# Performance work log

Hardware: AMD Instinct MI355X
Metric: run time of the kernel (lower is better)

The kernel has to match this reference:

```python
import jax, jax.numpy as jnp
import numpy as np

HD, M = 4096, 14336

def setup_inputs() -> dict:
    key = jax.random.key(0)
    k_x, k_g, k_u, k_d = jax.random.split(key, 4)
    scale = 1.0 / np.sqrt(HD)
    x = jax.random.normal(k_x, (4, 2048, HD), dtype=jnp.float16)
    # Dequantized fp16 weights, stored torch-style as [out_features, in_features]
    W_gate = (jax.random.normal(k_g, (M, HD), dtype=jnp.float16) * jnp.float16(scale))
    W_up   = (jax.random.normal(k_u, (M, HD), dtype=jnp.float16) * jnp.float16(scale))
    W_down = (jax.random.normal(k_d, (HD, M), dtype=jnp.float16) * jnp.float16(1.0 / np.sqrt(M)))
    return {"x": x, "W_gate": W_gate, "W_up": W_up, "W_down": W_down}

def reference(x, W_gate, W_up, W_down):
    # SwiGLU: down( silu(x @ Wg^T) * (x @ Wu^T) )
    gate = jnp.einsum("bsh,mh->bsm", x, W_gate)   # [B,S,M]
    up = jnp.einsum("bsh,mh->bsm", x, W_up)       # [B,S,M]
    h = jax.nn.silu(gate) * up                       # fused elementwise
    out = jnp.einsum("bsm,hm->bsh", h, W_down)    # [B,S,HD]
    return out
```

## Files before the change

kernel.cpp:

```cpp
#include <hip/hip_runtime.h>

typedef _Float16 f16;
typedef _Float16 f16x8 __attribute__((ext_vector_type(8)));
typedef float f32x4 __attribute__((ext_vector_type(4)));

__device__ __forceinline__ f16x8 cvt8(f32x4 lo, f32x4 hi) {
    f16x8 h;
    h[0] = (f16)lo[0]; h[1] = (f16)lo[1]; h[2] = (f16)lo[2]; h[3] = (f16)lo[3];
    h[4] = (f16)hi[0]; h[5] = (f16)hi[1]; h[6] = (f16)hi[2]; h[7] = (f16)hi[3];
    return h;
}

__global__ __launch_bounds__(256)
void cvt_f32_f16(const float* __restrict__ in, f16* __restrict__ out, long long n) {
    long long i = ((long long)blockIdx.x * 256 + threadIdx.x) * 8;
    const long long stride = (long long)gridDim.x * 256 * 8;
    for (; i < n; i += stride) {
        f32x4 a = *(const f32x4*)(in + i);
        f32x4 b = *(const f32x4*)(in + i + 4);
        *(f16x8*)(out + i) = cvt8(a, b);
    }
}

__global__ void fill_sentinel_f32(float* __restrict__ out, long long n) {
    long long i = (long long)blockIdx.x * blockDim.x + threadIdx.x;
    long long stride = (long long)gridDim.x * blockDim.x;
    for (; i < n; i += stride) out[i] = 1.0f;
}

__device__ __forceinline__ void gload_lds16(const f16* g, f16* l) {
    __builtin_amdgcn_global_load_lds(
        (const __attribute__((address_space(1))) unsigned int*)(unsigned long long)g,
        (__attribute__((address_space(3))) unsigned int*)(unsigned int)(unsigned long long)l,
        16, 0, 0);
}

template<int EPI>
__global__ __launch_bounds__(512, 2)
void mlp_gemm16c(const f16* __restrict__ A, const f16* __restrict__ B0,
                 void* __restrict__ Cv, int K, int ldc,
                 int nRow, int nCol, int RG) {
    __shared__ __align__(16) f16 smA[3][256 * 32];
    __shared__ __align__(16) f16 smB0[3][256 * 32];

    const int lin   = blockIdx.x;
    const int perSg = RG * nCol;
    const int sg    = lin / perSg;
    const int rem   = lin - sg * perSg;
    int rgIn = nRow - sg * RG; if (rgIn > RG) rgIn = RG;
    const int colB = rem / rgIn;
    const int rowB = sg * RG + (rem - colB * rgIn);

    const long long blockRow = (long long)rowB * 256;
    const long long blockCol = (long long)colB * 256;

    const int tid  = threadIdx.x;
    const int w    = tid >> 6;
    const int lane = tid & 63;
    const int waveM = w >> 2;
    const int waveN = w & 3;

    const int dr   = tid >> 2;
    const int dblk = tid & 3;
    const int gblk = (dblk - (dr >> 1)) & 3;
    const f16* gA0  = A  + (blockRow + dr) * (long long)K + gblk * 8;
    const f16* gA1  = gA0 + 128 * (long long)K;
    const f16* gB0a = B0 + (blockCol + dr) * (long long)K + gblk * 8;
    const f16* gB0b = gB0a + 128 * (long long)K;
    const int wbase = w * 512;

    const int fr = lane & 15;
    const int hi = lane >> 4;
    int aOff[8], bOff[4];
#pragma unroll
    for (int i = 0; i < 8; ++i) {
        const int r = waveM * 128 + i * 16 + fr;
        aOff[i] = r * 32 + (((hi + (r >> 1)) & 3) << 3);
    }
#pragma unroll
    for (int n = 0; n < 4; ++n) {
        const int r = waveN * 64 + n * 16 + fr;
        bOff[n] = r * 32 + (((hi + (r >> 1)) & 3) << 3);
    }

    f32x4 acc0[8][4];
#pragma unroll
    for (int mi = 0; mi < 8; ++mi)
#pragma unroll
        for (int ni = 0; ni < 4; ++ni)
            acc0[mi][ni] = (f32x4){0.f, 0.f, 0.f, 0.f};

    auto stage = [&](int b) {
        gload_lds16(gA0,  &smA[b][wbase]);           gA0  += 32;
        gload_lds16(gA1,  &smA[b][4096 + wbase]);    gA1  += 32;
        gload_lds16(gB0a, &smB0[b][wbase]);          gB0a += 32;
        gload_lds16(gB0b, &smB0[b][4096 + wbase]);   gB0b += 32;
    };

    auto compute = [&](int b) {
        f16x8 aF[8], bF[4];
#pragma unroll
        for (int i = 0; i < 8; ++i) aF[i] = *(const f16x8*)(&smA[b][aOff[i]]);
#pragma unroll
        for (int n = 0; n < 4; ++n) bF[n] = *(const f16x8*)(&smB0[b][bOff[n]]);
#pragma unroll
        for (int mi = 0; mi < 8; ++mi)
#pragma unroll
            for (int ni = 0; ni < 4; ++ni)
                acc0[mi][ni] = __builtin_amdgcn_mfma_f32_16x16x32_f16(
                    aF[mi], bF[ni], acc0[mi][ni], 0, 0, 0);
    };

    const int nk = K >> 5;
    stage(0);
    stage(1);
    int cur = 0;
    for (int t = 0; t < nk - 1; ++t) {
        asm volatile("s_waitcnt vmcnt(4)" ::: "memory");
        __builtin_amdgcn_s_barrier();
        __builtin_amdgcn_sched_barrier(0);
        if (t + 2 < nk) {
            int nb = cur + 2; if (nb >= 3) nb -= 3;
            stage(nb);
        }
        compute(cur);
        cur = (cur == 2) ? 0 : cur + 1;
    }
    asm volatile("s_waitcnt vmcnt(0)" ::: "memory");
    __builtin_amdgcn_s_barrier();
    __builtin_amdgcn_sched_barrier(0);
    compute(cur);

    const long long orBase = blockRow + waveM * 128 + hi * 4;
    const long long ocBase = blockCol + waveN * 64 + fr;
#pragma unroll
    for (int mi = 0; mi < 8; ++mi)
#pragma unroll
        for (int ni = 0; ni < 4; ++ni)
#pragma unroll
            for (int j = 0; j < 4; ++j) {
                const long long idx =
                    (orBase + mi * 16 + j) * (long long)ldc + (ocBase + ni * 16);
                float v = acc0[mi][ni][j];
                if constexpr (EPI == 0) {
                    ((float*)Cv)[idx] = v;
                } else if constexpr (EPI == 1) {
                    ((f16*)Cv)[idx] = (f16)(v / (1.f + __expf(-v)));
                } else {
                    f16* Hc = (f16*)Cv;
                    float h = (float)Hc[idx];
                    Hc[idx] = (f16)(h * v);
                }
            }
}

template<bool IS16>
__device__ __forceinline__ f16x8 load8(const char* p) {
    if constexpr (IS16) return *(const f16x8*)p;
    const float* f = (const float*)p;
    return cvt8(*(const f32x4*)f, *(const f32x4*)(f + 4));
}

template<bool FUSED, bool A16, bool B16>
__global__ __launch_bounds__(256)
void mlp_gemm(const void* __restrict__ Av, const void* __restrict__ B0v,
              const void* __restrict__ B1v, void* __restrict__ Cv,
              int K, int ldc, int nRow, int nCol, int RG) {
    __shared__ __align__(16) f16 smA[128 * 32];
    __shared__ __align__(16) f16 smB0[128 * 32];
    __shared__ __align__(16) f16 smB1[FUSED ? 128 * 32 : 8];

    const int lin   = blockIdx.x;
    const int perSg = RG * nCol;
    const int sg    = lin / perSg;
    const int rem   = lin - sg * perSg;
    int rgIn = nRow - sg * RG; if (rgIn > RG) rgIn = RG;
    const int colB = rem / rgIn;
    const int rowB = sg * RG + (rem - colB * rgIn);

    const long long blockRow = (long long)rowB * 128;
    const long long blockCol = (long long)colB * 128;

    const int tid  = threadIdx.x;
    const int w    = tid >> 6;
    const int lane = tid & 63;
    const int waveM = w >> 1;
    const int waveN = w & 1;

    const int r0 = tid >> 2;
    const int s0 = tid & 3;
    const int szA = A16 ? 2 : 4;
    const int szB = B16 ? 2 : 4;
    const char* gA0  = (const char*)Av  + ((blockRow + r0)      * (long long)K + s0 * 8) * szA;
    const char* gA1  = (const char*)Av  + ((blockRow + r0 + 64) * (long long)K + s0 * 8) * szA;
    const char* gB00 = (const char*)B0v + ((blockCol + r0)      * (long long)K + s0 * 8) * szB;
    const char* gB01 = (const char*)B0v + ((blockCol + r0 + 64) * (long long)K + s0 * 8) * szB;
    const char* gB10 = FUSED ? (const char*)B1v + ((blockCol + r0)      * (long long)K + s0 * 8) * szB : nullptr;
    const char* gB11 = FUSED ? (const char*)B1v + ((blockCol + r0 + 64) * (long long)K + s0 * 8) * szB : nullptr;

    const int off0 = tid * 8;
    const int off1 = off0 + 2048;

    const int fr = lane & 15;
    const int fk = (lane >> 4) * 8;
    int offA[4], offB[4];
#pragma unroll
    for (int i = 0; i < 4; ++i) {
        offA[i] = (waveM * 64 + i * 16 + fr) * 32 + fk;
        offB[i] = (waveN * 64 + i * 16 + fr) * 32 + fk;
    }

    f32x4 acc0[4][4];
    f32x4 acc1[4][4];
#pragma unroll
    for (int mi = 0; mi < 4; ++mi)
#pragma unroll
        for (int ni = 0; ni < 4; ++ni) {
            acc0[mi][ni] = (f32x4){0.f, 0.f, 0.f, 0.f};
            if constexpr (FUSED) acc1[mi][ni] = (f32x4){0.f, 0.f, 0.f, 0.f};
        }

    const int ksteps = K >> 5;
    for (int kt = 0; kt < ksteps; ++kt) {
        f16x8 vA0  = load8<A16>(gA0);
        f16x8 vA1  = load8<A16>(gA1);
        f16x8 vB00 = load8<B16>(gB00);
        f16x8 vB01 = load8<B16>(gB01);
        f16x8 vB10, vB11;
        if constexpr (FUSED) {
            vB10 = load8<B16>(gB10);
            vB11 = load8<B16>(gB11);
        }
        gA0 += 32 * szA; gA1 += 32 * szA;
        gB00 += 32 * szB; gB01 += 32 * szB;
        if constexpr (FUSED) { gB10 += 32 * szB; gB11 += 32 * szB; }

        __syncthreads();

        *(f16x8*)(smA  + off0) = vA0;
        *(f16x8*)(smA  + off1) = vA1;
        *(f16x8*)(smB0 + off0) = vB00;
        *(f16x8*)(smB0 + off1) = vB01;
        if constexpr (FUSED) {
            *(f16x8*)(smB1 + off0) = vB10;
            *(f16x8*)(smB1 + off1) = vB11;
        }

        __syncthreads();

        f16x8 aF[4], bF[4], b1F[4];
#pragma unroll
        for (int i = 0; i < 4; ++i) aF[i] = *(const f16x8*)(smA + offA[i]);
#pragma unroll
        for (int i = 0; i < 4; ++i) bF[i] = *(const f16x8*)(smB0 + offB[i]);
        if constexpr (FUSED) {
#pragma unroll
            for (int i = 0; i < 4; ++i) b1F[i] = *(const f16x8*)(smB1 + offB[i]);
        }

#pragma unroll
        for (int mi = 0; mi < 4; ++mi)
#pragma unroll
            for (int ni = 0; ni < 4; ++ni) {
                acc0[mi][ni] = __builtin_amdgcn_mfma_f32_16x16x32_f16(
                    aF[mi], bF[ni], acc0[mi][ni], 0, 0, 0);
                if constexpr (FUSED)
                    acc1[mi][ni] = __builtin_amdgcn_mfma_f32_16x16x32_f16(
                        aF[mi], b1F[ni], acc1[mi][ni], 0, 0, 0);
            }
    }

    const long long orBase = blockRow + waveM * 64 + ((lane >> 4) * 4);
    const long long ocBase = blockCol + waveN * 64 + fr;
#pragma unroll
    for (int mi = 0; mi < 4; ++mi)
#pragma unroll
        for (int ni = 0; ni < 4; ++ni)
#pragma unroll
            for (int j = 0; j < 4; ++j) {
                const long long idx =
                    (orBase + mi * 16 + j) * (long long)ldc + (ocBase + ni * 16);
                if constexpr (FUSED) {
                    float gv = acc0[mi][ni][j];
                    float uv = acc1[mi][ni][j];
                    float v = (gv / (1.f + __expf(-gv))) * uv;
                    ((f16*)Cv)[idx] = (f16)v;
                } else {
                    ((float*)Cv)[idx] = acc0[mi][ni][j];
                }
            }
}

extern "C" void kernel_launch(void* const* d_in, const int* in_sizes, int n_in,
                              void* d_out, int out_size, void* d_ws, size_t ws_size,
                              hipStream_t stream) {
    const float* x  = (const float*)d_in[0];
    const float* Wg = (const float*)d_in[1];
    const float* Wu = (const float*)d_in[2];
    const float* Wd = (const float*)d_in[3];
    float* out = (float*)d_out;

    const int HD = 4096;
    const int T  = in_sizes[0] / HD;
    const int M  = in_sizes[1] / HD;

    const long long nW = (long long)M * HD;
    const long long nX = (long long)T * HD;
    const size_t wBytes = (size_t)nW * 2;
    const size_t xBytes = (size_t)nX * 2;
    const size_t hRow   = (size_t)M * 2;
    const size_t minH   = 256 * hRow;

    char* p = (char*)d_ws;
    size_t rem = ws_size;
    f16 *Wg16 = nullptr, *Wu16 = nullptr, *Wd16 = nullptr, *X16 = nullptr;
    bool fast = false;
    if (rem >= 3 * wBytes + xBytes + minH) {
        Wg16 = (f16*)p; p += wBytes;
        Wu16 = (f16*)p; p += wBytes;
        Wd16 = (f16*)p; p += wBytes;
        X16  = (f16*)p; p += xBytes;
        rem -= 3 * wBytes + xBytes;
        fast = true;
    }
    f16* H = (f16*)p;

    if (fast) {
        long long maxRows = (long long)(rem / hRow);
        int chunk = (int)((maxRows / 256) * 256);
        if (chunk > T) chunk = T;

        cvt_f32_f16<<<2048, 256, 0, stream>>>(Wg, Wg16, nW);
        cvt_f32_f16<<<2048, 256, 0, stream>>>(Wu, Wu16, nW);
        cvt_f32_f16<<<2048, 256, 0, stream>>>(Wd, Wd16, nW);
        cvt_f32_f16<<<2048, 256, 0, stream>>>(x, X16, nX);

        const int nColGU = M / 256;
        const int nColD  = HD / 256;
        for (int t0 = 0; t0 < T; t0 += chunk) {
            int rows = (T - t0 < chunk) ? (T - t0) : chunk;
            int nRow = rows / 256;
            const f16* Xc = X16 + (size_t)t0 * HD;
            mlp_gemm16c<1><<<dim3(nRow * nColGU), 512, 0, stream>>>(
                Xc, Wg16, H, HD, M, nRow, nColGU, nRow);
            mlp_gemm16c<2><<<dim3(nRow * nColGU), 512, 0, stream>>>(
                Xc, Wu16, H, HD, M, nRow, nColGU, nRow);
            int RG = (nRow < 16) ? nRow : 16;
            mlp_gemm16c<0><<<dim3(nRow * nColD), 512, 0, stream>>>(
                H, Wd16, out + (size_t)t0 * HD, M, HD, nRow, nColD, RG);
        }
        return;
    }

    long long maxRows = (long long)(ws_size / hRow);
    int chunk = (int)((maxRows / 128) * 128);
    if (chunk > T) chunk = T;
    if (chunk <= 0) {
        fill_sentinel_f32<<<1024, 256, 0, stream>>>(out, (long long)out_size);
        return;
    }
    f16* Hf = (f16*)d_ws;
    for (int t0 = 0; t0 < T; t0 += chunk) {
        int rows = (T - t0 < chunk) ? (T - t0) : chunk;
        int nRow = rows / 128;
        {
            int nCol = M / 128;
            mlp_gemm<true, false, false><<<dim3(nRow * nCol), 256, 0, stream>>>(
                x + (size_t)t0 * HD, Wg, Wu, Hf, HD, M, nRow, nCol, nRow);
        }
        {
            int nCol = HD / 128;
            int RG = (nRow < 32) ? nRow : 32;
            mlp_gemm<false, true, false><<<dim3(nRow * nCol), 256, 0, stream>>>(
                Hf, Wd, nullptr, out + (size_t)t0 * HD, M, HD, nRow, nCol, RG);
        }
    }
}
```

Measured before the change: 2.930 ms.

## Fuse gate and up GEMMs via interleaved weight layout with SwiGLU epilogue

Interleaves the gate and up weight rows in blocks of 16 during the fp16 conversion, so a single GEMM over 2M output columns produces gate and up tiles side by side. The epilogue pairs adjacent 16-column fragments and applies silu(g)*u before writing H once. This removes the second GEMM launch, the read-modify-write of H, and the extra fp16 stores of the gate result. The cost is a more complex conversion kernel with strided source rows.

```diff
diff --git a/kernel.cpp b/kernel.cpp
--- a/kernel.cpp
+++ b/kernel.cpp
@@ -22,6 +22,21 @@
     }
 }
 
+__global__ __launch_bounds__(256)
+void cvt_interleave_f32_f16(const float* __restrict__ Wg,
+                            const float* __restrict__ Wu,
+                            f16* __restrict__ out, long long total) {
+    long long i = ((long long)blockIdx.x * 256 + threadIdx.x) * 8;
+    const long long stride = (long long)gridDim.x * 256 * 8;
+    for (; i < total; i += stride) {
+        const long long row = i >> 12;
+        const int col = (int)(i & 4095);
+        const long long srow = ((row >> 5) << 4) | (row & 15);
+        const float* src = ((row & 16) ? Wu : Wg) + srow * 4096 + col;
+        *(f16x8*)(out + i) = cvt8(*(const f32x4*)src, *(const f32x4*)(src + 4));
+    }
+}
+
 __global__ void fill_sentinel_f32(float* __restrict__ out, long long n) {
     long long i = (long long)blockIdx.x * blockDim.x + threadIdx.x;
     long long stride = (long long)gridDim.x * blockDim.x;
@@ -37,7 +52,7 @@
 
 template<int EPI>
 __global__ __launch_bounds__(512, 2)
-void mlp_gemm16c(const f16* __restrict__ A, const f16* __restrict__ B0,
+void mlp_gemm16d(const f16* __restrict__ A, const f16* __restrict__ B0,
                  void* __restrict__ Cv, int K, int ldc,
                  int nRow, int nCol, int RG) {
     __shared__ __align__(16) f16 smA[3][256 * 32];
@@ -132,26 +147,36 @@
     compute(cur);
 
     const long long orBase = blockRow + waveM * 128 + hi * 4;
-    const long long ocBase = blockCol + waveN * 64 + fr;
-#pragma unroll
-    for (int mi = 0; mi < 8; ++mi)
-#pragma unroll
-        for (int ni = 0; ni < 4; ++ni)
-#pragma unroll
-            for (int j = 0; j < 4; ++j) {
-                const long long idx =
-                    (orBase + mi * 16 + j) * (long long)ldc + (ocBase + ni * 16);
-                float v = acc0[mi][ni][j];
-                if constexpr (EPI == 0) {
-                    ((float*)Cv)[idx] = v;
-                } else if constexpr (EPI == 1) {
-                    ((f16*)Cv)[idx] = (f16)(v / (1.f + __expf(-v)));
-                } else {
-                    f16* Hc = (f16*)Cv;
-                    float h = (float)Hc[idx];
-                    Hc[idx] = (f16)(h * v);
+    if constexpr (EPI == 0) {
+        const long long ocBase = blockCol + waveN * 64 + fr;
+#pragma unroll
+        for (int mi = 0; mi < 8; ++mi)
+#pragma unroll
+            for (int ni = 0; ni < 4; ++ni)
+#pragma unroll
+                for (int j = 0; j < 4; ++j) {
+                    const long long idx =
+                        (orBase + mi * 16 + j) * (long long)ldc +
+                        (ocBase + ni * 16);
+                    ((float*)Cv)[idx] = acc0[mi][ni][j];
                 }
-            }
+    } else {
+        const long long ocBase = (blockCol >> 1) + waveN * 32 + fr;
+#pragma unroll
+        for (int mi = 0; mi < 8; ++mi)
+#pragma unroll
+            for (int pi = 0; pi < 2; ++pi)
+#pragma unroll
+                for (int j = 0; j < 4; ++j) {
+                    float g = acc0[mi][2 * pi][j];
+                    float u = acc0[mi][2 * pi + 1][j];
+                    float v = (g / (1.f + __expf(-g))) * u;
+                    const long long idx =
+                        (orBase + mi * 16 + j) * (long long)ldc +
+                        (ocBase + pi * 16);
+                    ((f16*)Cv)[idx] = (f16)v;
+                }
+    }
 }
 
 template<bool IS16>
@@ -313,11 +338,10 @@
 
     char* p = (char*)d_ws;
     size_t rem = ws_size;
-    f16 *Wg16 = nullptr, *Wu16 = nullptr, *Wd16 = nullptr, *X16 = nullptr;
+    f16 *Wgu = nullptr, *Wd16 = nullptr, *X16 = nullptr;
     bool fast = false;
     if (rem >= 3 * wBytes + xBytes + minH) {
-        Wg16 = (f16*)p; p += wBytes;
-        Wu16 = (f16*)p; p += wBytes;
+        Wgu  = (f16*)p; p += 2 * wBytes;
         Wd16 = (f16*)p; p += wBytes;
         X16  = (f16*)p; p += xBytes;
         rem -= 3 * wBytes + xBytes;
@@ -330,23 +354,19 @@
         int chunk = (int)((maxRows / 256) * 256);
         if (chunk > T) chunk = T;
 
-        cvt_f32_f16<<<2048, 256, 0, stream>>>(Wg, Wg16, nW);
-        cvt_f32_f16<<<2048, 256, 0, stream>>>(Wu, Wu16, nW);
+        cvt_interleave_f32_f16<<<2048, 256, 0, stream>>>(Wg, Wu, Wgu, 2 * nW);
         cvt_f32_f16<<<2048, 256, 0, stream>>>(Wd, Wd16, nW);
         cvt_f32_f16<<<2048, 256, 0, stream>>>(x, X16, nX);
 
-        const int nColGU = M / 256;
+        const int nColGU = (2 * M) / 256;
         const int nColD  = HD / 256;
         for (int t0 = 0; t0 < T; t0 += chunk) {
             int rows = (T - t0 < chunk) ? (T - t0) : chunk;
             int nRow = rows / 256;
-            const f16* Xc = X16 + (size_t)t0 * HD;
-            mlp_gemm16c<1><<<dim3(nRow * nColGU), 512, 0, stream>>>(
-                Xc, Wg16, H, HD, M, nRow, nColGU, nRow);
-            mlp_gemm16c<2><<<dim3(nRow * nColGU), 512, 0, stream>>>(
-                Xc, Wu16, H, HD, M, nRow, nColGU, nRow);
+            mlp_gemm16d<3><<<dim3(nRow * nColGU), 512, 0, stream>>>(
+                X16 + (size_t)t0 * HD, Wgu, H, HD, M, nRow, nColGU, nRow);
             int RG = (nRow < 16) ? nRow : 16;
-            mlp_gemm16c<0><<<dim3(nRow * nColD), 512, 0, stream>>>(
+            mlp_gemm16d<0><<<dim3(nRow * nColD), 512, 0, stream>>>(
                 H, Wd16, out + (size_t)t0 * HD, M, HD, nRow, nColD, RG);
         }
         return;
```

Measured after the change: 2.758 ms (median of 4 runs). -5.9%, faster.
